# Kernel tuning notes

Hardware: AMD Instinct MI355X
Metric: run time of the kernel (lower is better)

The kernel has to match this reference:

```python
import jax, jax.numpy as jnp
import numpy as np

B, S, D, H = 2, 2048, 1024, 16
DK = D // H  # 64


def setup_inputs() -> dict:
    key = jax.random.key(0)
    ks = jax.random.split(key, 9)
    query = jax.random.normal(ks[0], (B, S, D), dtype=jnp.float32)
    k_in = jax.random.normal(ks[1], (B, S, D), dtype=jnp.float32)
    v_in = jax.random.normal(ks[2], (B, S, D), dtype=jnp.float32)
    mask = jax.random.randint(ks[3], (B, S, S), 0, 2, dtype=jnp.int32)
    sc = 1.0 / np.sqrt(D)
    Wq = jax.random.normal(ks[4], (H, D, DK), dtype=jnp.float32) * sc  # per-head q proj
    Wk = jax.random.normal(ks[5], (H, D, DK), dtype=jnp.float32) * sc
    Wv = jax.random.normal(ks[6], (H, D, DK), dtype=jnp.float32) * sc
    Wu = jax.random.normal(ks[7], (D, D), dtype=jnp.float32) * sc  # unifyheads weight
    bu = jax.random.normal(ks[8], (D,), dtype=jnp.float32) * 0.01
    return {"query": query, "key": k_in, "value": v_in, "mask": mask,
            "Wq": Wq, "Wk": Wk, "Wv": Wv, "Wu": Wu, "bu": bu}


def reference(query, key, value, mask, Wq, Wk, Wv, Wu, bu):
    scale = DK ** 0.25  # original divides q and k each by d_k^(1/4)
    q = jnp.einsum('bsd,hdk->bhsk', query, Wq) / scale
    k = jnp.einsum('bsd,hdk->bhsk', key, Wk) / scale
    v = jnp.einsum('bsd,hdk->bhsk', value, Wv)
    scores = jnp.einsum('bhsk,bhtk->bhst', q, k)  # [B,H,S,S]
    scores = jnp.where(mask[:, None, :, :] == 0, jnp.float32(-1e9), scores)
    attn = jax.nn.softmax(scores, axis=-1)
    out = jnp.einsum('bhst,bhtk->bhsk', attn, v)
    out = jnp.transpose(out, (0, 2, 1, 3)).reshape(query.shape[0], query.shape[1], D)  # concat heads
    return out @ Wu + bu
```

## Files before the change

### kernel.cpp

```cpp
#include <hip/hip_runtime.h>
#include <hip/hip_bf16.h>


typedef __bf16 bf16_t;
typedef __attribute__((ext_vector_type(4))) __bf16 bf16x4;
typedef __attribute__((ext_vector_type(8))) __bf16 bf16x8;
typedef __attribute__((ext_vector_type(4))) float f32x4;
typedef unsigned int u32;

#define B_ 2
#define S_ 2048
#define D_ 1024
#define H_ 16
#define DK_ 64
#define NX_ (4096 * 1024)

static __device__ __forceinline__ f32x4 mfma16(bf16x8 a, bf16x8 b, f32x4 c) {
  return __builtin_amdgcn_mfma_f32_16x16x32_bf16(a, b, c, 0, 0, 0);
}

static __device__ __forceinline__ void async16(const bf16_t* g, bf16_t* l) {
  __builtin_amdgcn_global_load_lds(
      (const __attribute__((address_space(1))) u32*)g,
      (__attribute__((address_space(3))) u32*)l, 16, 0, 0);
}

__global__ __launch_bounds__(256) void cvt_x(const float* __restrict__ q,
                                             const float* __restrict__ k,
                                             const float* __restrict__ v,
                                             bf16_t* __restrict__ qo,
                                             bf16_t* __restrict__ ko,
                                             bf16_t* __restrict__ vo) {
  const int z = blockIdx.y;
  const float* src = (z == 0) ? q : (z == 1) ? k : v;
  bf16_t* dst = (z == 0) ? qo : (z == 1) ? ko : vo;
  size_t i = ((size_t)blockIdx.x * 256 + threadIdx.x) * 8;
  float4 a = *(const float4*)(src + i);
  float4 b = *(const float4*)(src + i + 4);
  bf16x8 o;
  o[0] = (bf16_t)a.x; o[1] = (bf16_t)a.y; o[2] = (bf16_t)a.z; o[3] = (bf16_t)a.w;
  o[4] = (bf16_t)b.x; o[5] = (bf16_t)b.y; o[6] = (bf16_t)b.z; o[7] = (bf16_t)b.w;
  *(bf16x8*)(dst + i) = o;
}

__global__ __launch_bounds__(256) void wtrans(
    const float* __restrict__ Wq, const float* __restrict__ Wk,
    const float* __restrict__ Wv, const float* __restrict__ Wu,
    bf16_t* __restrict__ Bq, bf16_t* __restrict__ Bk,
    bf16_t* __restrict__ Bv, bf16_t* __restrict__ Bu, float qkscale) {
  __shared__ __align__(16) bf16_t T[64][72];
  const int z = blockIdx.z;
  const float* W = (z == 0) ? Wq : (z == 1) ? Wk : (z == 2) ? Wv : Wu;
  bf16_t* BT = (z == 0) ? Bq : (z == 1) ? Bk : (z == 2) ? Bv : Bu;
  const float scale = (z <= 1) ? qkscale : 1.0f;
  const int d0 = blockIdx.x * 64, nt = blockIdx.y;
  const int tid = threadIdx.x;
  const int r = tid & 63, g = tid >> 6;

  const float* src = (z < 3)
      ? W + ((size_t)nt * D_ + d0 + r) * DK_ + g * 16
      : W + (size_t)(d0 + r) * D_ + nt * 64 + g * 16;
#pragma unroll
  for (int j = 0; j < 4; ++j) {
    float4 w4 = *(const float4*)(src + j * 4);
    T[g * 16 + j * 4 + 0][r] = (bf16_t)(w4.x * scale);
    T[g * 16 + j * 4 + 1][r] = (bf16_t)(w4.y * scale);
    T[g * 16 + j * 4 + 2][r] = (bf16_t)(w4.z * scale);
    T[g * 16 + j * 4 + 3][r] = (bf16_t)(w4.w * scale);
  }
  __syncthreads();
  const int orow = tid >> 3, seg = tid & 7;
#pragma unroll
  for (int p = 0; p < 2; ++p) {
    int rr = p * 32 + orow;
    *(bf16x8*)(BT + (size_t)(nt * 64 + rr) * D_ + d0 + seg * 8) =
        *(const bf16x8*)&T[rr][seg * 8];
  }
}

__global__ __launch_bounds__(256) void vt_build(const bf16_t* __restrict__ V,
                                                bf16_t* __restrict__ Vt) {
  __shared__ __align__(16) bf16_t T[64][72];
  const int r0 = blockIdx.x * 64;
  const int c0 = blockIdx.y * 64;
  const int tid = threadIdx.x;
#pragma unroll
  for (int it = 0; it < 2; ++it) {
    int t = tid + it * 256;
    int rr = t >> 3, cc = (t & 7) * 8;
    *(bf16x8*)&T[rr][cc] = *(const bf16x8*)(V + (size_t)(r0 + rr) * D_ + c0 + cc);
  }
  __syncthreads();
#pragma unroll
  for (int it = 0; it < 2; ++it) {
    int t = tid + it * 256;
    int cr = t >> 3, rc = (t & 7) * 8;
    bf16x8 v;
#pragma unroll
    for (int j = 0; j < 8; ++j) v[j] = T[rc + j][cr];
    *(bf16x8*)(Vt + (size_t)(c0 + cr) * 4096 + r0 + rc) = v;
  }
}

__global__ __launch_bounds__(256) void mask_pack(const int* __restrict__ mask,
                                                 unsigned int* __restrict__ bits) {
  int w = blockIdx.x * 256 + threadIdx.x;
  const int4* p = (const int4*)(mask + (size_t)w * 32);
  unsigned int v = 0;
#pragma unroll
  for (int i = 0; i < 8; ++i) {
    int4 m4 = p[i];
    v |= (m4.x != 0 ? 1u : 0u) << (i * 4 + 0);
    v |= (m4.y != 0 ? 1u : 0u) << (i * 4 + 1);
    v |= (m4.z != 0 ? 1u : 0u) << (i * 4 + 2);
    v |= (m4.w != 0 ? 1u : 0u) << (i * 4 + 3);
  }
  bits[w] = v;
}

__global__ __launch_bounds__(256) void gemm_bt(
    const bf16_t* __restrict__ A0, const bf16_t* __restrict__ A1,
    const bf16_t* __restrict__ A2, const bf16_t* __restrict__ BT0,
    const bf16_t* __restrict__ BT1, const bf16_t* __restrict__ BT2,
    bf16_t* __restrict__ C0, bf16_t* __restrict__ C1, bf16_t* __restrict__ C2) {
  __shared__ __align__(16) bf16_t As[128 * 64];
  __shared__ __align__(16) bf16_t Bs[128 * 64];

  const int z = blockIdx.z;
  const bf16_t* A = (z == 0) ? A0 : (z == 1) ? A1 : A2;
  const bf16_t* BT = (z == 0) ? BT0 : (z == 1) ? BT1 : BT2;
  bf16_t* C = (z == 0) ? C0 : (z == 1) ? C1 : C2;

  const int tid = threadIdx.x;
  const int lane = tid & 63, wave = tid >> 6;
  const int l = lane & 15, quad = lane >> 4;
  const int wm = wave >> 1, wn = wave & 1;
  const int row0 = blockIdx.x * 128, col0 = blockIdx.y * 128;

  const int lr = lane >> 3;
  const int gc8 = (lane & 7) ^ lr;
  const int xl = l & 7;

  f32x4 acc[4][4];
#pragma unroll
  for (int i = 0; i < 4; ++i)
#pragma unroll
    for (int j = 0; j < 4; ++j) acc[i][j] = {0.f, 0.f, 0.f, 0.f};

  for (int k0 = 0; k0 < 1024; k0 += 64) {
    __syncthreads();
#pragma unroll
    for (int c = 0; c < 4; ++c) {
      int r = wave * 32 + c * 8;
      async16(A + (size_t)(row0 + r + lr) * 1024 + k0 + gc8 * 8, As + r * 64);
      async16(BT + (size_t)(col0 + r + lr) * 1024 + k0 + gc8 * 8, Bs + r * 64);
    }
    __syncthreads();

#pragma unroll
    for (int kh = 0; kh < 2; ++kh) {
      bf16x8 af[4], bf[4];
#pragma unroll
      for (int f = 0; f < 4; ++f)
        af[f] = *(const bf16x8*)&As[(wm * 64 + f * 16 + l) * 64 +
                                    (((kh * 4 + quad) ^ xl) * 8)];
#pragma unroll
      for (int f = 0; f < 4; ++f)
        bf[f] = *(const bf16x8*)&Bs[(wn * 64 + f * 16 + l) * 64 +
                                    (((kh * 4 + quad) ^ xl) * 8)];
#pragma unroll
      for (int fm = 0; fm < 4; ++fm)
#pragma unroll
        for (int fn = 0; fn < 4; ++fn)
          acc[fm][fn] = mfma16(af[fm], bf[fn], acc[fm][fn]);
    }
  }

#pragma unroll
  for (int fm = 0; fm < 4; ++fm)
#pragma unroll
    for (int fn = 0; fn < 4; ++fn)
#pragma unroll
      for (int reg = 0; reg < 4; ++reg) {
        int row = row0 + wm * 64 + fm * 16 + quad * 4 + reg;
        int col = col0 + wn * 64 + fn * 16 + l;
        C[(size_t)row * 1024 + col] = (bf16_t)acc[fm][fn][reg];
      }
}

__global__ __launch_bounds__(256) void gemm_bt64(
    const bf16_t* __restrict__ A, const bf16_t* __restrict__ BT,
    float* __restrict__ C, const float* __restrict__ bias) {
  __shared__ __align__(16) bf16_t As[64 * 64];
  __shared__ __align__(16) bf16_t Bs[128 * 64];

  const int tid = threadIdx.x;
  const int lane = tid & 63, wave = tid >> 6;
  const int l = lane & 15, quad = lane >> 4;
  const int row0 = blockIdx.x * 64, col0 = blockIdx.y * 128;

  const int lr = lane >> 3;
  const int gc8 = (lane & 7) ^ lr;
  const int xl = l & 7;

  f32x4 acc[4][2];
#pragma unroll
  for (int i = 0; i < 4; ++i)
#pragma unroll
    for (int j = 0; j < 2; ++j) acc[i][j] = {0.f, 0.f, 0.f, 0.f};

  for (int k0 = 0; k0 < 1024; k0 += 64) {
    __syncthreads();
#pragma unroll
    for (int c = 0; c < 2; ++c) {
      int r = wave * 16 + c * 8;
      async16(A + (size_t)(row0 + r + lr) * 1024 + k0 + gc8 * 8, As + r * 64);
    }
#pragma unroll
    for (int c = 0; c < 4; ++c) {
      int r = wave * 32 + c * 8;
      async16(BT + (size_t)(col0 + r + lr) * 1024 + k0 + gc8 * 8, Bs + r * 64);
    }
    __syncthreads();

#pragma unroll
    for (int kh = 0; kh < 2; ++kh) {
      bf16x8 af[4], bf[2];
#pragma unroll
      for (int f = 0; f < 4; ++f)
        af[f] = *(const bf16x8*)&As[(f * 16 + l) * 64 +
                                    (((kh * 4 + quad) ^ xl) * 8)];
#pragma unroll
      for (int f = 0; f < 2; ++f)
        bf[f] = *(const bf16x8*)&Bs[(wave * 32 + f * 16 + l) * 64 +
                                    (((kh * 4 + quad) ^ xl) * 8)];
#pragma unroll
      for (int fm = 0; fm < 4; ++fm)
#pragma unroll
        for (int fn = 0; fn < 2; ++fn)
          acc[fm][fn] = mfma16(af[fm], bf[fn], acc[fm][fn]);
    }
  }

#pragma unroll
  for (int fm = 0; fm < 4; ++fm)
#pragma unroll
    for (int fn = 0; fn < 2; ++fn)
#pragma unroll
      for (int reg = 0; reg < 4; ++reg) {
        int row = row0 + fm * 16 + quad * 4 + reg;
        int col = col0 + wave * 32 + fn * 16 + l;
        C[(size_t)row * 1024 + col] = acc[fm][fn][reg] + bias[col];
      }
}

__global__ __launch_bounds__(128) void attn_kernel(
    const bf16_t* __restrict__ Qx, const bf16_t* __restrict__ Kx,
    const bf16_t* __restrict__ Vt, const unsigned int* __restrict__ mbits,
    bf16_t* __restrict__ out) {
  __shared__ __align__(16) bf16_t Ks[64 * 64];
  __shared__ __align__(16) bf16_t Vts[64 * 64];
  __shared__ __align__(16) bf16_t Ps[2][32][72];

  const int tid = threadIdx.x;
  const int lane = tid & 63, wave = tid >> 6;
  const int l = lane & 15, quad = lane >> 4;
  const int qt = blockIdx.x, h = blockIdx.y, b = blockIdx.z;
  const int ch = h * 64;
  const size_t rb = (size_t)b * S_;
  const int q0 = qt * 64 + wave * 32;

  const int lr = lane >> 3;
  const int gc8 = (lane & 7) ^ lr;
  const int xl = l & 7;

  bf16x8 bq[2][2];
#pragma unroll
  for (int mf = 0; mf < 2; ++mf) {
    const bf16_t* qp = Qx + (rb + q0 + mf * 16 + l) * D_ + ch;
    bq[mf][0] = *(const bf16x8*)(qp + quad * 8);
    bq[mf][1] = *(const bf16x8*)(qp + 32 + quad * 8);
  }

  const f32x4 zero = {0.f, 0.f, 0.f, 0.f};
  f32x4 o[2][4];
  float lsum[2] = {0.f, 0.f};
#pragma unroll
  for (int mf = 0; mf < 2; ++mf)
#pragma unroll
    for (int nt = 0; nt < 4; ++nt) o[mf][nt] = zero;

  const u32* mrow[2];
#pragma unroll
  for (int mf = 0; mf < 2; ++mf)
    mrow[mf] = mbits + (size_t)(b * S_ + q0 + mf * 16 + l) * (S_ / 32);

  for (int t0 = 0; t0 < S_; t0 += 64) {
    __syncthreads();
#pragma unroll
    for (int it = 0; it < 4; ++it) {
      int r0 = it * 16 + wave * 8;
      async16(Kx + (rb + t0 + r0 + lr) * D_ + ch + gc8 * 8, Ks + r0 * 64);
      async16(Vt + (size_t)(ch + r0 + lr) * 4096 + rb + t0 + gc8 * 8,
              Vts + r0 * 64);
    }
    __syncthreads();

#pragma unroll
    for (int mf = 0; mf < 2; ++mf) {
      u32 mw0 = mrow[mf][(t0 >> 5)];
      u32 mw1 = mrow[mf][(t0 >> 5) + 1];
#pragma unroll
      for (int ts = 0; ts < 4; ++ts) {
        int rK = (ts * 16 + l) * 64;
        bf16x8 ak0 = *(const bf16x8*)&Ks[rK + ((quad ^ xl) * 8)];
        bf16x8 ak1 = *(const bf16x8*)&Ks[rK + (((4 + quad) ^ xl) * 8)];
        f32x4 s = mfma16(ak0, bq[mf][0], zero);
        s = mfma16(ak1, bq[mf][1], s);

        u32 mw = (ts < 2) ? mw0 : mw1;
        u32 nib = (mw >> ((ts & 1) * 16 + quad * 4)) & 0xFu;
        bf16x4 pv;
#pragma unroll
        for (int reg = 0; reg < 4; ++reg) {
          float e = __expf(fminf(s[reg], 30.0f));
          float p = ((nib >> reg) & 1u) ? e : 0.0f;
          lsum[mf] += p;
          pv[reg] = (bf16_t)p;
        }
        *(bf16x4*)&Ps[wave][mf * 16 + l][ts * 16 + quad * 4] = pv;
      }
    }

    bf16x8 ap[2][2];
#pragma unroll
    for (int mf = 0; mf < 2; ++mf) {
      ap[mf][0] = *(const bf16x8*)&Ps[wave][mf * 16 + l][quad * 8];
      ap[mf][1] = *(const bf16x8*)&Ps[wave][mf * 16 + l][32 + quad * 8];
    }
#pragma unroll
    for (int nt = 0; nt < 4; ++nt) {
      int rV = (nt * 16 + l) * 64;
      bf16x8 bv0 = *(const bf16x8*)&Vts[rV + ((quad ^ xl) * 8)];
      bf16x8 bv1 = *(const bf16x8*)&Vts[rV + (((4 + quad) ^ xl) * 8)];
#pragma unroll
      for (int mf = 0; mf < 2; ++mf) {
        o[mf][nt] = mfma16(ap[mf][0], bv0, o[mf][nt]);
        o[mf][nt] = mfma16(ap[mf][1], bv1, o[mf][nt]);
      }
    }
  }

#pragma unroll
  for (int mf = 0; mf < 2; ++mf) {
    float rsum = lsum[mf];
    rsum += __shfl_xor(rsum, 16);
    rsum += __shfl_xor(rsum, 32);
    float inv = (rsum > 0.f) ? (1.f / rsum) : 0.f;
    float invr[4];
#pragma unroll
    for (int reg = 0; reg < 4; ++reg) invr[reg] = __shfl(inv, quad * 4 + reg);
#pragma unroll
    for (int reg = 0; reg < 4; ++reg) {
      int srow = q0 + mf * 16 + quad * 4 + reg;
      bf16_t* op = out + (rb + srow) * D_ + ch;
#pragma unroll
      for (int nt = 0; nt < 4; ++nt)
        op[nt * 16 + l] = (bf16_t)(o[mf][nt][reg] * invr[reg]);
    }
  }
}

extern "C" void kernel_launch(void* const* d_in, const int* in_sizes, int n_in,
                              void* d_out, int out_size, void* d_ws, size_t ws_size,
                              hipStream_t stream) {
  const float* q_in = (const float*)d_in[0];
  const float* k_in = (const float*)d_in[1];
  const float* v_in = (const float*)d_in[2];
  const int* mask = (const int*)d_in[3];
  const float* Wq = (const float*)d_in[4];
  const float* Wk = (const float*)d_in[5];
  const float* Wv = (const float*)d_in[6];
  const float* Wu = (const float*)d_in[7];
  const float* bu = (const float*)d_in[8];
  float* outp = (float*)d_out;

  bf16_t* qx = (bf16_t*)d_ws;
  bf16_t* kx = qx + NX_;
  bf16_t* vx = kx + NX_;
  bf16_t* qb = vx + NX_;
  bf16_t* kb = qb + NX_;
  bf16_t* vb = kb + NX_;
  bf16_t* BTq = vb + NX_;
  bf16_t* BTk = BTq + D_ * D_;
  bf16_t* BTv = BTk + D_ * D_;
  bf16_t* BTu = BTv + D_ * D_;
  unsigned int* mb = (unsigned int*)(BTu + D_ * D_);
  bf16_t* ab = qx;
  bf16_t* vtb = kx;

  const float qkscale = 0.35355339059327373f;

  dim3 blk(256);
  cvt_x<<<dim3(2048, 3), blk, 0, stream>>>(q_in, k_in, v_in, qx, kx, vx);
  wtrans<<<dim3(16, 16, 4), blk, 0, stream>>>(Wq, Wk, Wv, Wu, BTq, BTk, BTv, BTu, qkscale);
  mask_pack<<<dim3(1024), blk, 0, stream>>>(mask, mb);
  gemm_bt<<<dim3(32, 8, 3), blk, 0, stream>>>(qx, kx, vx, BTq, BTk, BTv,
                                              qb, kb, vb);
  vt_build<<<dim3(64, 16), blk, 0, stream>>>(vb, vtb);
  attn_kernel<<<dim3(S_ / 64, H_, B_), dim3(128), 0, stream>>>(qb, kb, vtb, mb, ab);
  gemm_bt64<<<dim3(64, 8), blk, 0, stream>>>(ab, BTu, outp, bu);
}
```

Measured before the change: 287.3 us.

## Split attention key range across two wave pairs with LDS reduction

The attention kernel now launches 256 threads per block. Two wave pairs each process half of every 128-key chunk for the same 64 query rows, and the partial outputs and row sums are combined through shared memory at the end. This halves the number of sequential key-loop iterations per wave and adds more waves per block to hide latency. In exchange it uses more LDS per block and adds a final reduction and extra barriers. The global load per barrier interval doubles, and each wave now issues eight loads of either K or V only.

```diff
diff --git a/kernel.cpp b/kernel.cpp
--- a/kernel.cpp
+++ b/kernel.cpp
@@ -254,21 +254,21 @@
       }
 }
 
-__global__ __launch_bounds__(128) void attn_kernel(
+__global__ __launch_bounds__(256) void attn_kernel(
     const bf16_t* __restrict__ Qx, const bf16_t* __restrict__ Kx,
     const bf16_t* __restrict__ Vt, const unsigned int* __restrict__ mbits,
     bf16_t* __restrict__ out) {
-  __shared__ __align__(16) bf16_t Ks[64 * 64];
-  __shared__ __align__(16) bf16_t Vts[64 * 64];
-  __shared__ __align__(16) bf16_t Ps[2][32][72];
+  __shared__ __align__(16) bf16_t KVs[4][64 * 64];
+  __shared__ __align__(16) bf16_t Ps[4][32][72];
 
   const int tid = threadIdx.x;
   const int lane = tid & 63, wave = tid >> 6;
   const int l = lane & 15, quad = lane >> 4;
+  const int qh = wave & 1, p = wave >> 1;
   const int qt = blockIdx.x, h = blockIdx.y, b = blockIdx.z;
   const int ch = h * 64;
   const size_t rb = (size_t)b * S_;
-  const int q0 = qt * 64 + wave * 32;
+  const int q0 = qt * 64 + qh * 32;
 
   const int lr = lane >> 3;
   const int gc8 = (lane & 7) ^ lr;
@@ -295,26 +295,33 @@
   for (int mf = 0; mf < 2; ++mf)
     mrow[mf] = mbits + (size_t)(b * S_ + q0 + mf * 16 + l) * (S_ / 32);
 
-  for (int t0 = 0; t0 < S_; t0 += 64) {
-    __syncthreads();
-#pragma unroll
-    for (int it = 0; it < 4; ++it) {
-      int r0 = it * 16 + wave * 8;
-      async16(Kx + (rb + t0 + r0 + lr) * D_ + ch + gc8 * 8, Ks + r0 * 64);
-      async16(Vt + (size_t)(ch + r0 + lr) * 4096 + rb + t0 + gc8 * 8,
-              Vts + r0 * 64);
-    }
-    __syncthreads();
-
+  const bf16_t* Kp = KVs[p];
+  const bf16_t* Vp = KVs[2 + p];
+
+  for (int t0 = 0; t0 < S_; t0 += 128) {
+    __syncthreads();
+#pragma unroll
+    for (int j = 0; j < 8; ++j) {
+      int r0 = j * 8;
+      if (wave < 2)
+        async16(Kx + (rb + t0 + qh * 64 + r0 + lr) * D_ + ch + gc8 * 8,
+                KVs[wave] + r0 * 64);
+      else
+        async16(Vt + (size_t)(ch + r0 + lr) * 4096 + rb + t0 + qh * 64 + gc8 * 8,
+                KVs[wave] + r0 * 64);
+    }
+    __syncthreads();
+
+    const int tw = t0 + p * 64;
 #pragma unroll
     for (int mf = 0; mf < 2; ++mf) {
-      u32 mw0 = mrow[mf][(t0 >> 5)];
-      u32 mw1 = mrow[mf][(t0 >> 5) + 1];
+      u32 mw0 = mrow[mf][(tw >> 5)];
+      u32 mw1 = mrow[mf][(tw >> 5) + 1];
 #pragma unroll
       for (int ts = 0; ts < 4; ++ts) {
         int rK = (ts * 16 + l) * 64;
-        bf16x8 ak0 = *(const bf16x8*)&Ks[rK + ((quad ^ xl) * 8)];
-        bf16x8 ak1 = *(const bf16x8*)&Ks[rK + (((4 + quad) ^ xl) * 8)];
+        bf16x8 ak0 = *(const bf16x8*)&Kp[rK + ((quad ^ xl) * 8)];
+        bf16x8 ak1 = *(const bf16x8*)&Kp[rK + (((4 + quad) ^ xl) * 8)];
         f32x4 s = mfma16(ak0, bq[mf][0], zero);
         s = mfma16(ak1, bq[mf][1], s);
 
@@ -324,9 +331,9 @@
 #pragma unroll
         for (int reg = 0; reg < 4; ++reg) {
           float e = __expf(fminf(s[reg], 30.0f));
-          float p = ((nib >> reg) & 1u) ? e : 0.0f;
-          lsum[mf] += p;
-          pv[reg] = (bf16_t)p;
+          float pp = ((nib >> reg) & 1u) ? e : 0.0f;
+          lsum[mf] += pp;
+          pv[reg] = (bf16_t)pp;
         }
         *(bf16x4*)&Ps[wave][mf * 16 + l][ts * 16 + quad * 4] = pv;
       }
@@ -341,8 +348,8 @@
 #pragma unroll
     for (int nt = 0; nt < 4; ++nt) {
       int rV = (nt * 16 + l) * 64;
-      bf16x8 bv0 = *(const bf16x8*)&Vts[rV + ((quad ^ xl) * 8)];
-      bf16x8 bv1 = *(const bf16x8*)&Vts[rV + (((4 + quad) ^ xl) * 8)];
+      bf16x8 bv0 = *(const bf16x8*)&Vp[rV + ((quad ^ xl) * 8)];
+      bf16x8 bv1 = *(const bf16x8*)&Vp[rV + (((4 + quad) ^ xl) * 8)];
 #pragma unroll
       for (int mf = 0; mf < 2; ++mf) {
         o[mf][nt] = mfma16(ap[mf][0], bv0, o[mf][nt]);
@@ -351,22 +358,47 @@
     }
   }
 
-#pragma unroll
-  for (int mf = 0; mf < 2; ++mf) {
-    float rsum = lsum[mf];
-    rsum += __shfl_xor(rsum, 16);
-    rsum += __shfl_xor(rsum, 32);
-    float inv = (rsum > 0.f) ? (1.f / rsum) : 0.f;
-    float invr[4];
-#pragma unroll
-    for (int reg = 0; reg < 4; ++reg) invr[reg] = __shfl(inv, quad * 4 + reg);
-#pragma unroll
-    for (int reg = 0; reg < 4; ++reg) {
-      int srow = q0 + mf * 16 + quad * 4 + reg;
-      bf16_t* op = out + (rb + srow) * D_ + ch;
+  __syncthreads();
+  float* Sm = (float*)KVs;
+  const int mrow36 = (qh * 64 + lane) * 36;
+  if (p == 1) {
+#pragma unroll
+    for (int mf = 0; mf < 2; ++mf) {
 #pragma unroll
       for (int nt = 0; nt < 4; ++nt)
-        op[nt * 16 + l] = (bf16_t)(o[mf][nt][reg] * invr[reg]);
+        *(f32x4*)&Sm[mrow36 + (mf * 4 + nt) * 4] = o[mf][nt];
+      Sm[mrow36 + 32 + mf] = lsum[mf];
+    }
+  }
+  __syncthreads();
+  if (p == 0) {
+#pragma unroll
+    for (int mf = 0; mf < 2; ++mf) {
+#pragma unroll
+      for (int nt = 0; nt < 4; ++nt) {
+        f32x4 t = *(const f32x4*)&Sm[mrow36 + (mf * 4 + nt) * 4];
+#pragma unroll
+        for (int r = 0; r < 4; ++r) o[mf][nt][r] += t[r];
+      }
+      lsum[mf] += Sm[mrow36 + 32 + mf];
+    }
+#pragma unroll
+    for (int mf = 0; mf < 2; ++mf) {
+      float rsum = lsum[mf];
+      rsum += __shfl_xor(rsum, 16);
+      rsum += __shfl_xor(rsum, 32);
+      float inv = (rsum > 0.f) ? (1.f / rsum) : 0.f;
+      float invr[4];
+#pragma unroll
+      for (int reg = 0; reg < 4; ++reg) invr[reg] = __shfl(inv, quad * 4 + reg);
+#pragma unroll
+      for (int reg = 0; reg < 4; ++reg) {
+        int srow = q0 + mf * 16 + quad * 4 + reg;
+        bf16_t* op = out + (rb + srow) * D_ + ch;
+#pragma unroll
+        for (int nt = 0; nt < 4; ++nt)
+          op[nt * 16 + l] = (bf16_t)(o[mf][nt][reg] * invr[reg]);
+      }
     }
   }
 }
@@ -408,6 +440,6 @@
   gemm_bt<<<dim3(32, 8, 3), blk, 0, stream>>>(qx, kx, vx, BTq, BTk, BTv,
                                               qb, kb, vb);
   vt_build<<<dim3(64, 16), blk, 0, stream>>>(vb, vtb);
-  attn_kernel<<<dim3(S_ / 64, H_, B_), dim3(128), 0, stream>>>(qb, kb, vtb, mb, ab);
+  attn_kernel<<<dim3(S_ / 64, H_, B_), blk, 0, stream>>>(qb, kb, vtb, mb, ab);
   gemm_bt64<<<dim3(64, 8), blk, 0, stream>>>(ab, BTu, outp, bu);
 }
```

New measurement: 288.0 us. About the same (+0.3%).

## Split attention key range across two blocks and merge partials; fuse prep kernels

Applied to the files above, without the earlier changes.

The attention kernel now splits the key sequence into two halves, each handled by its own block. Each block writes unnormalized partial outputs and row sums, and a new merge kernel adds the halves and normalizes. This doubles the number of attention blocks from 1024 to 2048 to improve GPU occupancy, at the cost of extra global traffic for the partials and one more launch. Separately, the input conversion, weight transpose and mask packing kernels are fused into a single prep launch to cut launch overhead.

```diff
diff --git a/kernel.cpp b/kernel.cpp
--- a/kernel.cpp
+++ b/kernel.cpp
@@ -25,56 +25,69 @@
       (__attribute__((address_space(3))) u32*)l, 16, 0, 0);
 }
 
-__global__ __launch_bounds__(256) void cvt_x(const float* __restrict__ q,
-                                             const float* __restrict__ k,
-                                             const float* __restrict__ v,
-                                             bf16_t* __restrict__ qo,
-                                             bf16_t* __restrict__ ko,
-                                             bf16_t* __restrict__ vo) {
-  const int z = blockIdx.y;
-  const float* src = (z == 0) ? q : (z == 1) ? k : v;
-  bf16_t* dst = (z == 0) ? qo : (z == 1) ? ko : vo;
-  size_t i = ((size_t)blockIdx.x * 256 + threadIdx.x) * 8;
-  float4 a = *(const float4*)(src + i);
-  float4 b = *(const float4*)(src + i + 4);
-  bf16x8 o;
-  o[0] = (bf16_t)a.x; o[1] = (bf16_t)a.y; o[2] = (bf16_t)a.z; o[3] = (bf16_t)a.w;
-  o[4] = (bf16_t)b.x; o[5] = (bf16_t)b.y; o[6] = (bf16_t)b.z; o[7] = (bf16_t)b.w;
-  *(bf16x8*)(dst + i) = o;
-}
-
-__global__ __launch_bounds__(256) void wtrans(
+__global__ __launch_bounds__(256) void prep(
+    const float* __restrict__ q, const float* __restrict__ k,
+    const float* __restrict__ v, const int* __restrict__ mask,
     const float* __restrict__ Wq, const float* __restrict__ Wk,
     const float* __restrict__ Wv, const float* __restrict__ Wu,
+    bf16_t* __restrict__ qo, bf16_t* __restrict__ ko, bf16_t* __restrict__ vo,
     bf16_t* __restrict__ Bq, bf16_t* __restrict__ Bk,
-    bf16_t* __restrict__ Bv, bf16_t* __restrict__ Bu, float qkscale) {
+    bf16_t* __restrict__ Bv, bf16_t* __restrict__ Bu,
+    u32* __restrict__ bits, float qkscale) {
   __shared__ __align__(16) bf16_t T[64][72];
-  const int z = blockIdx.z;
-  const float* W = (z == 0) ? Wq : (z == 1) ? Wk : (z == 2) ? Wv : Wu;
-  bf16_t* BT = (z == 0) ? Bq : (z == 1) ? Bk : (z == 2) ? Bv : Bu;
-  const float scale = (z <= 1) ? qkscale : 1.0f;
-  const int d0 = blockIdx.x * 64, nt = blockIdx.y;
-  const int tid = threadIdx.x;
-  const int r = tid & 63, g = tid >> 6;
-
-  const float* src = (z < 3)
-      ? W + ((size_t)nt * D_ + d0 + r) * DK_ + g * 16
-      : W + (size_t)(d0 + r) * D_ + nt * 64 + g * 16;
-#pragma unroll
-  for (int j = 0; j < 4; ++j) {
-    float4 w4 = *(const float4*)(src + j * 4);
-    T[g * 16 + j * 4 + 0][r] = (bf16_t)(w4.x * scale);
-    T[g * 16 + j * 4 + 1][r] = (bf16_t)(w4.y * scale);
-    T[g * 16 + j * 4 + 2][r] = (bf16_t)(w4.z * scale);
-    T[g * 16 + j * 4 + 3][r] = (bf16_t)(w4.w * scale);
-  }
-  __syncthreads();
-  const int orow = tid >> 3, seg = tid & 7;
-#pragma unroll
-  for (int p = 0; p < 2; ++p) {
-    int rr = p * 32 + orow;
-    *(bf16x8*)(BT + (size_t)(nt * 64 + rr) * D_ + d0 + seg * 8) =
-        *(const bf16x8*)&T[rr][seg * 8];
+  const int y = blockIdx.y, x = blockIdx.x, tid = threadIdx.x;
+
+  if (y < 3) {
+    const float* src = (y == 0) ? q : (y == 1) ? k : v;
+    bf16_t* dst = (y == 0) ? qo : (y == 1) ? ko : vo;
+    size_t i = ((size_t)x * 256 + tid) * 8;
+    float4 a = *(const float4*)(src + i);
+    float4 b = *(const float4*)(src + i + 4);
+    bf16x8 o;
+    o[0] = (bf16_t)a.x; o[1] = (bf16_t)a.y; o[2] = (bf16_t)a.z; o[3] = (bf16_t)a.w;
+    o[4] = (bf16_t)b.x; o[5] = (bf16_t)b.y; o[6] = (bf16_t)b.z; o[7] = (bf16_t)b.w;
+    *(bf16x8*)(dst + i) = o;
+  } else if (y == 3) {
+    if (x >= 1024) return;
+    const int z = x >> 8;
+    const float* W = (z == 0) ? Wq : (z == 1) ? Wk : (z == 2) ? Wv : Wu;
+    bf16_t* BT = (z == 0) ? Bq : (z == 1) ? Bk : (z == 2) ? Bv : Bu;
+    const float scale = (z <= 1) ? qkscale : 1.0f;
+    const int d0 = (x & 15) * 64, nt = (x >> 4) & 15;
+    const int r = tid & 63, g = tid >> 6;
+    const float* src = (z < 3)
+        ? W + ((size_t)nt * D_ + d0 + r) * DK_ + g * 16
+        : W + (size_t)(d0 + r) * D_ + nt * 64 + g * 16;
+#pragma unroll
+    for (int j = 0; j < 4; ++j) {
+      float4 w4 = *(const float4*)(src + j * 4);
+      T[g * 16 + j * 4 + 0][r] = (bf16_t)(w4.x * scale);
+      T[g * 16 + j * 4 + 1][r] = (bf16_t)(w4.y * scale);
+      T[g * 16 + j * 4 + 2][r] = (bf16_t)(w4.z * scale);
+      T[g * 16 + j * 4 + 3][r] = (bf16_t)(w4.w * scale);
+    }
+    __syncthreads();
+    const int orow = tid >> 3, seg = tid & 7;
+#pragma unroll
+    for (int p = 0; p < 2; ++p) {
+      int rr = p * 32 + orow;
+      *(bf16x8*)(BT + (size_t)(nt * 64 + rr) * D_ + d0 + seg * 8) =
+          *(const bf16x8*)&T[rr][seg * 8];
+    }
+  } else {
+    if (x >= 1024) return;
+    int w = x * 256 + tid;
+    const int4* p = (const int4*)(mask + (size_t)w * 32);
+    u32 v2 = 0;
+#pragma unroll
+    for (int i = 0; i < 8; ++i) {
+      int4 m4 = p[i];
+      v2 |= (m4.x != 0 ? 1u : 0u) << (i * 4 + 0);
+      v2 |= (m4.y != 0 ? 1u : 0u) << (i * 4 + 1);
+      v2 |= (m4.z != 0 ? 1u : 0u) << (i * 4 + 2);
+      v2 |= (m4.w != 0 ? 1u : 0u) << (i * 4 + 3);
+    }
+    bits[w] = v2;
   }
 }
 
@@ -100,22 +113,6 @@
     for (int j = 0; j < 8; ++j) v[j] = T[rc + j][cr];
     *(bf16x8*)(Vt + (size_t)(c0 + cr) * 4096 + r0 + rc) = v;
   }
-}
-
-__global__ __launch_bounds__(256) void mask_pack(const int* __restrict__ mask,
-                                                 unsigned int* __restrict__ bits) {
-  int w = blockIdx.x * 256 + threadIdx.x;
-  const int4* p = (const int4*)(mask + (size_t)w * 32);
-  unsigned int v = 0;
-#pragma unroll
-  for (int i = 0; i < 8; ++i) {
-    int4 m4 = p[i];
-    v |= (m4.x != 0 ? 1u : 0u) << (i * 4 + 0);
-    v |= (m4.y != 0 ? 1u : 0u) << (i * 4 + 1);
-    v |= (m4.z != 0 ? 1u : 0u) << (i * 4 + 2);
-    v |= (m4.w != 0 ? 1u : 0u) << (i * 4 + 3);
-  }
-  bits[w] = v;
 }
 
 __global__ __launch_bounds__(256) void gemm_bt(
@@ -256,8 +253,9 @@
 
 __global__ __launch_bounds__(128) void attn_kernel(
     const bf16_t* __restrict__ Qx, const bf16_t* __restrict__ Kx,
-    const bf16_t* __restrict__ Vt, const unsigned int* __restrict__ mbits,
-    bf16_t* __restrict__ out) {
+    const bf16_t* __restrict__ Vt, const u32* __restrict__ mbits,
+    bf16_t* __restrict__ po0, bf16_t* __restrict__ po1,
+    float* __restrict__ ls) {
   __shared__ __align__(16) bf16_t Ks[64 * 64];
   __shared__ __align__(16) bf16_t Vts[64 * 64];
   __shared__ __align__(16) bf16_t Ps[2][32][72];
@@ -265,10 +263,12 @@
   const int tid = threadIdx.x;
   const int lane = tid & 63, wave = tid >> 6;
   const int l = lane & 15, quad = lane >> 4;
-  const int qt = blockIdx.x, h = blockIdx.y, b = blockIdx.z;
+  const int qt = blockIdx.x >> 1, split = blockIdx.x & 1;
+  const int h = blockIdx.y, b = blockIdx.z;
   const int ch = h * 64;
   const size_t rb = (size_t)b * S_;
   const int q0 = qt * 64 + wave * 32;
+  const int tbeg = split * (S_ / 2), tend = tbeg + S_ / 2;
 
   const int lr = lane >> 3;
   const int gc8 = (lane & 7) ^ lr;
@@ -295,7 +295,7 @@
   for (int mf = 0; mf < 2; ++mf)
     mrow[mf] = mbits + (size_t)(b * S_ + q0 + mf * 16 + l) * (S_ / 32);
 
-  for (int t0 = 0; t0 < S_; t0 += 64) {
+  for (int t0 = tbeg; t0 < tend; t0 += 64) {
     __syncthreads();
 #pragma unroll
     for (int it = 0; it < 4; ++it) {
@@ -324,9 +324,9 @@
 #pragma unroll
         for (int reg = 0; reg < 4; ++reg) {
           float e = __expf(fminf(s[reg], 30.0f));
-          float p = ((nib >> reg) & 1u) ? e : 0.0f;
-          lsum[mf] += p;
-          pv[reg] = (bf16_t)p;
+          float pp = ((nib >> reg) & 1u) ? e : 0.0f;
+          lsum[mf] += pp;
+          pv[reg] = (bf16_t)pp;
         }
         *(bf16x4*)&Ps[wave][mf * 16 + l][ts * 16 + quad * 4] = pv;
       }
@@ -351,24 +351,42 @@
     }
   }
 
+  bf16_t* po = split ? po1 : po0;
 #pragma unroll
   for (int mf = 0; mf < 2; ++mf) {
     float rsum = lsum[mf];
     rsum += __shfl_xor(rsum, 16);
     rsum += __shfl_xor(rsum, 32);
-    float inv = (rsum > 0.f) ? (1.f / rsum) : 0.f;
-    float invr[4];
-#pragma unroll
-    for (int reg = 0; reg < 4; ++reg) invr[reg] = __shfl(inv, quad * 4 + reg);
+    if (quad == 0)
+      ls[(size_t)split * (B_ * S_ * H_) + (rb + q0 + mf * 16 + l) * H_ + h] = rsum;
 #pragma unroll
     for (int reg = 0; reg < 4; ++reg) {
       int srow = q0 + mf * 16 + quad * 4 + reg;
-      bf16_t* op = out + (rb + srow) * D_ + ch;
+      bf16_t* op = po + (rb + srow) * D_ + ch;
 #pragma unroll
       for (int nt = 0; nt < 4; ++nt)
-        op[nt * 16 + l] = (bf16_t)(o[mf][nt][reg] * invr[reg]);
-    }
-  }
+        op[nt * 16 + l] = (bf16_t)o[mf][nt][reg];
+    }
+  }
+}
+
+__global__ __launch_bounds__(256) void attn_merge(
+    const bf16_t* __restrict__ po0, const bf16_t* __restrict__ po1,
+    const float* __restrict__ ls, bf16_t* __restrict__ ab) {
+  int idx = blockIdx.x * 256 + threadIdx.x;
+  int r = idx >> 7;
+  int c8 = (idx & 127) * 8;
+  int hh = c8 >> 6;
+  float l0 = ls[(size_t)r * H_ + hh];
+  float l1 = ls[(size_t)(B_ * S_ * H_) + (size_t)r * H_ + hh];
+  float sum = l0 + l1;
+  float inv = (sum > 0.f) ? (1.f / sum) : 0.f;
+  bf16x8 a = *(const bf16x8*)(po0 + (size_t)r * D_ + c8);
+  bf16x8 b = *(const bf16x8*)(po1 + (size_t)r * D_ + c8);
+  bf16x8 o;
+#pragma unroll
+  for (int j = 0; j < 8; ++j) o[j] = (bf16_t)(((float)a[j] + (float)b[j]) * inv);
+  *(bf16x8*)(ab + (size_t)r * D_ + c8) = o;
 }
 
 extern "C" void kernel_launch(void* const* d_in, const int* in_sizes, int n_in,
@@ -395,19 +413,24 @@
   bf16_t* BTk = BTq + D_ * D_;
   bf16_t* BTv = BTk + D_ * D_;
   bf16_t* BTu = BTv + D_ * D_;
-  unsigned int* mb = (unsigned int*)(BTu + D_ * D_);
+  u32* mb = (u32*)(BTu + D_ * D_);
+  float* ls = (float*)(mb + B_ * S_ * S_ / 32);
   bf16_t* ab = qx;
   bf16_t* vtb = kx;
+  bf16_t* po0 = vx;
+  bf16_t* po1 = vb;
 
   const float qkscale = 0.35355339059327373f;
 
   dim3 blk(256);
-  cvt_x<<<dim3(2048, 3), blk, 0, stream>>>(q_in, k_in, v_in, qx, kx, vx);
-  wtrans<<<dim3(16, 16, 4), blk, 0, stream>>>(Wq, Wk, Wv, Wu, BTq, BTk, BTv, BTu, qkscale);
-  mask_pack<<<dim3(1024), blk, 0, stream>>>(mask, mb);
+  prep<<<dim3(2048, 5), blk, 0, stream>>>(q_in, k_in, v_in, mask, Wq, Wk, Wv, Wu,
+                                          qx, kx, vx, BTq, BTk, BTv, BTu, mb,
+                                          qkscale);
   gemm_bt<<<dim3(32, 8, 3), blk, 0, stream>>>(qx, kx, vx, BTq, BTk, BTv,
                                               qb, kb, vb);
   vt_build<<<dim3(64, 16), blk, 0, stream>>>(vb, vtb);
-  attn_kernel<<<dim3(S_ / 64, H_, B_), dim3(128), 0, stream>>>(qb, kb, vtb, mb, ab);
+  attn_kernel<<<dim3(S_ / 32, H_, B_), dim3(128), 0, stream>>>(qb, kb, vtb, mb,
+                                                               po0, po1, ls);
+  attn_merge<<<dim3(2048), blk, 0, stream>>>(po0, po1, ls, ab);
   gemm_bt64<<<dim3(64, 8), blk, 0, stream>>>(ab, BTu, outp, bu);
 }
```

Measured after the change: 289.6 us. About the same (+0.8%).
